# Kernel tuning notes

Measured on AMD Instinct MI355X. Metric: run time of the kernel, lower is better.

The kernel has to match this reference:

```python
import jax, jax.numpy as jnp
import numpy as np


def setup_inputs() -> dict:
    key = jax.random.key(0)
    k1, k2, k3, k4 = jax.random.split(key, 4)
    B, h, w, z, C = 4, 16, 16, 16, 128
    Cq = C // 8
    x = jax.random.normal(k1, (B, h, w, z, C), dtype=jnp.float32)
    # 1x1x1 Conv3D kernels == per-voxel linear projections (he_normal scale)
    Wb = jax.random.normal(k2, (C, Cq), dtype=jnp.float32) * np.sqrt(2.0 / C)
    Wc = jax.random.normal(k3, (C, Cq), dtype=jnp.float32) * np.sqrt(2.0 / C)
    Wd = jax.random.normal(k4, (C, C), dtype=jnp.float32) * np.sqrt(2.0 / C)
    gamma = jnp.zeros((1,), dtype=jnp.float32)
    return {"x": x, "Wb": Wb, "Wc": Wc, "Wd": Wd, "gamma": gamma}


def reference(x, Wb, Wc, Wd, gamma):
    B, h, w, z, C = x.shape
    N = h * w * z
    # 1x1x1 convs = channel projections
    b = jnp.einsum('bhwzc,cf->bhwzf', x, Wb).reshape(B, N, -1)   # [B,N,C/8]
    c = jnp.einsum('bhwzc,cf->bhwzf', x, Wc).reshape(B, N, -1)   # [B,N,C/8]
    d = jnp.einsum('bhwzc,cf->bhwzf', x, Wd).reshape(B, N, C)    # [B,N,C]
    # full NxN attention scores, softmax over last axis (keras softmax default)
    scores = jnp.einsum('bnf,bmf->bnm', b, c)                    # [B,N,N]
    attn = jax.nn.softmax(scores, axis=-1)
    out = jnp.einsum('bnm,bmc->bnc', attn, d).reshape(B, h, w, z, C)
    return gamma * out + x
```

## Files before the change

kernel.cpp:

```cpp
#include <hip/hip_runtime.h>

#define NB     4
#define NN     4096
#define NC     128
#define NCQ    16
#define NROWS  (NB * NN)
#define NSLICE 4
#define NIT    (NN / 64 / NSLICE)

typedef __attribute__((ext_vector_type(8)))  __bf16 bf16x8;
typedef __attribute__((ext_vector_type(4)))  float  f32x4;
typedef __attribute__((ext_vector_type(16))) float  f32x16;

#define MFMA16(a,b,c) __builtin_amdgcn_mfma_f32_16x16x32_bf16((a),(b),(c),0,0,0)
#define MFMA32(a,b,c) __builtin_amdgcn_mfma_f32_32x32x16_bf16((a),(b),(c),0,0,0)
#define LOG2E 1.44269504f
#define SCH_BIAS 16248.66f

__device__ __forceinline__ f32x16 zero16() {
    f32x16 v;
    #pragma unroll
    for (int i = 0; i < 16; ++i) v[i] = 0.f;
    return v;
}


__global__ void wtrans_kernel(const float* __restrict__ Wb,
                              const float* __restrict__ Wc,
                              const float* __restrict__ Wd,
                              __bf16* __restrict__ wtg)
{
    int oc = blockIdx.x;
    int ch = threadIdx.x;
    float v;
    if      (oc < 16) v = Wb[ch * 16  + oc];
    else if (oc < 32) v = Wc[ch * 16  + (oc - 16)];
    else              v = Wd[ch * 128 + (oc - 32)];
    wtg[oc * 128 + ch] = (__bf16)v;
}

__global__ __launch_bounds__(256) void proj_kernel(
    const float* __restrict__ x, const __bf16* __restrict__ wtg,
    __bf16* __restrict__ qswz, __bf16* __restrict__ kswz, __bf16* __restrict__ vswz)
{
    __shared__ __align__(16) __bf16 xsh[32 * 136];
    __shared__ __align__(16) __bf16 wt [160 * 136];
    __shared__ __align__(16) float  osb[4][16 * 17];

    const int  t    = threadIdx.x;
    const int  lane = t & 63, w = t >> 6;
    const int  q16  = lane & 15, quad = lane >> 4;
    const long row0 = (long)blockIdx.x * 32;
    const int  batch = (int)(row0 >> 12);
    const int  nloc  = (int)(row0 & 4095);
    const int  rh   = w & 1;
    const int  og   = (w >> 1) * 5;

    #pragma unroll
    for (int i = 0; i < 4; ++i) {
        int idx = t + 256 * i;
        int r = idx >> 5, c4 = (idx & 31) * 4;
        float4 xv = *(const float4*)&x[(row0 + r) * NC + c4];
        union { __bf16 h[4]; uint2 u; } cv;
        cv.h[0] = (__bf16)xv.x; cv.h[1] = (__bf16)xv.y;
        cv.h[2] = (__bf16)xv.z; cv.h[3] = (__bf16)xv.w;
        *(uint2*)&xsh[r * 136 + c4] = cv.u;
    }
    #pragma unroll
    for (int i = 0; i < 10; ++i) {
        int idx = t + 256 * i;
        int oc = idx >> 4, seg = idx & 15;
        *(uint4*)&wt[oc * 136 + seg * 8] = ((const uint4*)wtg)[idx];
    }
    __syncthreads();

    bf16x8 xf[4];
    #pragma unroll
    for (int kc = 0; kc < 4; ++kc)
        xf[kc] = *(const bf16x8*)&xsh[(rh * 16 + q16) * 136 + kc * 32 + quad * 8];

    float* osw = osb[w];
    #pragma unroll
    for (int oc_t = 0; oc_t < 5; ++oc_t) {
        const int oset = og + oc_t;
        f32x4 acc = {0.f, 0.f, 0.f, 0.f};
        #pragma unroll
        for (int kc = 0; kc < 4; ++kc) {
            bf16x8 wf = *(const bf16x8*)&wt[(oset * 16 + q16) * 136 + kc * 32 + quad * 8];
            acc = MFMA16(wf, xf[kc], acc);
        }
        #pragma unroll
        for (int r = 0; r < 4; ++r)
            osw[(quad * 4 + r) * 17 + q16] = acc[r];

        if (oset >= 2) {
            int ch_l = lane & 15, lh_t = (lane >> 4) & 1, jh = lane >> 5;
            union { __bf16 h[4]; uint2 u; } cv;
            #pragma unroll
            for (int u2 = 0; u2 < 4; ++u2)
                cv.h[u2] = (__bf16)osw[ch_l * 17 + 8 * jh + 4 * lh_t + u2];
            int kb16 = (nloc >> 4) + rh;
            int cg   = (oset - 2) >> 1;
            int l31v = ((oset - 2) & 1) * 16 + ch_l;
            size_t off = ((((size_t)batch * 256 + kb16) * 4 + cg) << 9)
                       + (size_t)(lh_t * 32 + l31v) * 8 + jh * 4;
            *(uint2*)&vswz[off] = cv.u;
        } else if (lane < 32) {
            int xr = lane & 15, lh_t = lane >> 4;
            const float qsc = (oset == 0) ? LOG2E : 1.f;
            union { __bf16 h[8]; uint4 u; } cv;
            #pragma unroll
            for (int j = 0; j < 8; ++j)
                cv.h[j] = (__bf16)(osw[(8 * lh_t + j) * 17 + xr] * qsc);
            size_t off = ((((size_t)batch * 128 + (nloc >> 5)) * 64)
                       + (size_t)(lh_t * 32 + rh * 16 + xr)) * 8;
            __bf16* dst = (oset == 0) ? qswz : kswz;
            *(uint4*)&dst[off] = cv.u;
        }
    }
}

__global__ __launch_bounds__(256, 3) void attn_kernel(
    const __bf16* __restrict__ qswz, const __bf16* __restrict__ kswz,
    const __bf16* __restrict__ vswz, __bf16* __restrict__ Opart,
    float* __restrict__ lws)
{
    const int t    = threadIdx.x;
    const int lane = t & 63, w = t >> 6;
    const int l31 = lane & 31, lh = lane >> 5;
    const int bid   = blockIdx.x;
    const int xcd   = bid & 7;
    const int batch = xcd >> 1;
    const int sp    = xcd & 1;
    const int qb32  = bid >> 3;
    const int h     = w & 1;
    const int slice = sp * 2 + (w >> 1);
    const int ks0   = slice * (64 * NIT);

    const bf16x8 qf = *(const bf16x8*)
        &qswz[(((size_t)batch * 128 + qb32) * 64 + lane) * 8];

    const __bf16* kptr = kswz + ((size_t)batch * 128 + (ks0 >> 5)) * 512 + lane * 8;
    const __bf16* vptr = vswz + ((size_t)batch * 256 + (ks0 >> 4)) * 2048
                       + h * 1024 + lane * 8;

    union { uint32_t u[4]; bf16x8 f; } onesu;
    #pragma unroll
    for (int i = 0; i < 4; ++i) onesu.u[i] = 0x3F803F80u;
    const bf16x8 ones = onesu.f;

    f32x16 O0 = zero16(), O1 = zero16(), Ol = zero16();

    bf16x8 kf0 = *(const bf16x8*)(kptr);
    bf16x8 kf1 = *(const bf16x8*)(kptr + 512);
    bf16x8 va[8], vb[8];
    #pragma unroll
    for (int b = 0; b < 4; ++b) {
        va[2*b]     = *(const bf16x8*)(vptr + (size_t)(b * 4)     * 512);
        va[2*b + 1] = *(const bf16x8*)(vptr + (size_t)(b * 4 + 1) * 512);
    }
    f32x16 S0 = MFMA32(kf0, qf, zero16());
    f32x16 S1 = MFMA32(kf1, qf, zero16());

#define ATTN_BODY(IT, CUR, NXT)                                               \
    {                                                                         \
        const int itn = ((IT) + 1 < NIT) ? (IT) + 1 : (IT);                   \
        kf0 = *(const bf16x8*)(kptr + (size_t)itn * 1024);                    \
        kf1 = *(const bf16x8*)(kptr + (size_t)itn * 1024 + 512);              \
        _Pragma("unroll")                                                     \
        for (int b = 0; b < 4; ++b) {                                         \
            NXT[2*b]     = *(const bf16x8*)(vptr + (size_t)((itn*4+b)*4)*512);\
            NXT[2*b + 1] = *(const bf16x8*)(vptr + (size_t)((itn*4+b)*4+1)*512);\
        }                                                                     \
        union { uint32_t u32[16]; bf16x8 f[4]; } pk;                          \
        _Pragma("unroll")                                                     \
        for (int i = 0; i < 8; ++i) {                                         \
            int e0 = (int)fmaf(S0[2*i],   128.f, SCH_BIAS);                   \
            int e1 = (int)fmaf(S0[2*i+1], 128.f, SCH_BIAS);                   \
            int e2 = (int)fmaf(S1[2*i],   128.f, SCH_BIAS);                   \
            int e3 = (int)fmaf(S1[2*i+1], 128.f, SCH_BIAS);                   \
            pk.u32[i]     = (uint32_t)((e1 << 16) | e0);                      \
            pk.u32[8 + i] = (uint32_t)((e3 << 16) | e2);                      \
        }                                                                     \
        _Pragma("unroll")                                                     \
        for (int b = 0; b < 4; ++b) {                                         \
            O0 = MFMA32(pk.f[b], CUR[2*b],     O0);                           \
            O1 = MFMA32(pk.f[b], CUR[2*b + 1], O1);                           \
            Ol = MFMA32(pk.f[b], ones,         Ol);                           \
        }                                                                     \
        S0 = MFMA32(kf0, qf, zero16());                                       \
        S1 = MFMA32(kf1, qf, zero16());                                       \
    }

    for (int it = 0; it < NIT; it += 2) {
        ATTN_BODY(it,     va, vb);
        ATTN_BODY(it + 1, vb, va);
    }
#undef ATTN_BODY

    const long base = (long)batch * NN;

    if (h == 0 && l31 == 0) {
        #pragma unroll
        for (int r = 0; r < 16; ++r) {
            int q = qb32 * 32 + (r & 3) + 8 * (r >> 2) + 4 * lh;
            lws[(size_t)slice * NROWS + base + q] = Ol[r];
        }
    }

    #pragma unroll
    for (int ct = 0; ct < 2; ++ct) {
        f32x16 Ov = ct ? O1 : O0;
        #pragma unroll
        for (int r = 0; r < 16; ++r) {
            int q = qb32 * 32 + (r & 3) + 8 * (r >> 2) + 4 * lh;
            Opart[((size_t)slice * NROWS + base + q) * NC + 64 * h + 32 * ct + l31]
                = (__bf16)Ov[r];
        }
    }
}

__global__ __launch_bounds__(256) void combine_kernel(
    const __bf16* __restrict__ Op, const float* __restrict__ lws,
    const float* __restrict__ x, const float* __restrict__ gamma,
    float* __restrict__ out)
{
    __shared__ float gl[32];
    const int  t    = threadIdx.x;
    const long row0 = (long)blockIdx.x * 32;
    if (t < 32) {
        float l = 0.f;
        #pragma unroll
        for (int s = 0; s < NSLICE; ++s) l += lws[(size_t)s * NROWS + row0 + t];
        gl[t] = gamma[0] / l;
    }
    __syncthreads();
    const size_t s1 = (size_t)NROWS * NC;
    #pragma unroll
    for (int i = 0; i < 4; ++i) {
        int idx = t + 256 * i;
        int r = idx >> 5, c4 = (idx & 31) * 4;
        size_t g = (size_t)(row0 + r) * NC + c4;
        float a0 = 0.f, a1 = 0.f, a2 = 0.f, a3 = 0.f;
        #pragma unroll
        for (int s = 0; s < NSLICE; ++s) {
            union { __bf16 h[4]; uint2 u; } a;
            a.u = *(const uint2*)&Op[s1 * s + g];
            a0 += (float)a.h[0]; a1 += (float)a.h[1];
            a2 += (float)a.h[2]; a3 += (float)a.h[3];
        }
        float sc = gl[r];
        float4 xv = *(const float4*)&x[g];
        float4 o;
        o.x = a0 * sc + xv.x; o.y = a1 * sc + xv.y;
        o.z = a2 * sc + xv.z; o.w = a3 * sc + xv.w;
        *(float4*)&out[g] = o;
    }
}

extern "C" void kernel_launch(void* const* d_in, const int* in_sizes, int n_in,
                              void* d_out, int out_size, void* d_ws, size_t ws_size,
                              hipStream_t stream) {
    const float* x     = (const float*)d_in[0];
    const float* Wb    = (const float*)d_in[1];
    const float* Wc    = (const float*)d_in[2];
    const float* Wd    = (const float*)d_in[3];
    const float* gamma = (const float*)d_in[4];
    float*       out   = (float*)d_out;

    __bf16* qswz  = (__bf16*)d_ws;
    __bf16* kswz  = qswz + (size_t)NROWS * NCQ;
    __bf16* vswz  = kswz + (size_t)NROWS * NCQ;
    __bf16* wtg   = vswz + (size_t)NB * NC * NN;
    __bf16* Opart = wtg + 160 * 128;
    float*  lws   = (float*)(Opart + (size_t)NSLICE * NROWS * NC);

    wtrans_kernel <<<160, 128, 0, stream>>>(Wb, Wc, Wd, wtg);
    proj_kernel   <<<NROWS / 32, 256, 0, stream>>>(x, wtg, qswz, kswz, vswz);
    attn_kernel   <<<NB * 128 * 2, 256, 0, stream>>>(qswz, kswz, vswz, Opart, lws);
    combine_kernel<<<NROWS / 32, 256, 0, stream>>>(Opart, lws, x, gamma, out);
}
```

Before: 112.8 us.

## Fuse weight transpose into projection and combine into attention via completion counter

Removes the separate weight-transpose kernel: each projection block now reads the fp32 weights directly and transposes and converts them into shared memory. The combine kernel is also removed. Each attention block bumps a per-query-tile atomic counter after writing its partials, and the second block to finish reduces the slices and writes the output. This cuts the launch count from four to two at the cost of redundant weight loads per projection block, strided shared-memory stores, and an atomic plus fences in the attention epilogue.

```diff
diff --git a/kernel.cpp b/kernel.cpp
--- a/kernel.cpp
+++ b/kernel.cpp
@@ -25,23 +25,11 @@
 }
 
 
-__global__ void wtrans_kernel(const float* __restrict__ Wb,
-                              const float* __restrict__ Wc,
-                              const float* __restrict__ Wd,
-                              __bf16* __restrict__ wtg)
-{
-    int oc = blockIdx.x;
-    int ch = threadIdx.x;
-    float v;
-    if      (oc < 16) v = Wb[ch * 16  + oc];
-    else if (oc < 32) v = Wc[ch * 16  + (oc - 16)];
-    else              v = Wd[ch * 128 + (oc - 32)];
-    wtg[oc * 128 + ch] = (__bf16)v;
-}
-
 __global__ __launch_bounds__(256) void proj_kernel(
-    const float* __restrict__ x, const __bf16* __restrict__ wtg,
-    __bf16* __restrict__ qswz, __bf16* __restrict__ kswz, __bf16* __restrict__ vswz)
+    const float* __restrict__ x,  const float* __restrict__ Wb,
+    const float* __restrict__ Wc, const float* __restrict__ Wd,
+    __bf16* __restrict__ qswz, __bf16* __restrict__ kswz,
+    __bf16* __restrict__ vswz, int* __restrict__ cnt)
 {
     __shared__ __align__(16) __bf16 xsh[32 * 136];
     __shared__ __align__(16) __bf16 wt [160 * 136];
@@ -56,6 +44,8 @@
     const int  rh   = w & 1;
     const int  og   = (w >> 1) * 5;
 
+    if (t == 0) cnt[blockIdx.x] = 0;
+
     #pragma unroll
     for (int i = 0; i < 4; ++i) {
         int idx = t + 256 * i;
@@ -67,10 +57,34 @@
         *(uint2*)&xsh[r * 136 + c4] = cv.u;
     }
     #pragma unroll
-    for (int i = 0; i < 10; ++i) {
+    for (int i = 0; i < 2; ++i) {
         int idx = t + 256 * i;
-        int oc = idx >> 4, seg = idx & 15;
-        *(uint4*)&wt[oc * 136 + seg * 8] = ((const uint4*)wtg)[idx];
+        int ch = idx >> 2, o4 = (idx & 3) * 4;
+        float4 v = *(const float4*)&Wb[ch * 16 + o4];
+        wt[(o4 + 0) * 136 + ch] = (__bf16)v.x;
+        wt[(o4 + 1) * 136 + ch] = (__bf16)v.y;
+        wt[(o4 + 2) * 136 + ch] = (__bf16)v.z;
+        wt[(o4 + 3) * 136 + ch] = (__bf16)v.w;
+    }
+    #pragma unroll
+    for (int i = 0; i < 2; ++i) {
+        int idx = t + 256 * i;
+        int ch = idx >> 2, o4 = (idx & 3) * 4;
+        float4 v = *(const float4*)&Wc[ch * 16 + o4];
+        wt[(16 + o4 + 0) * 136 + ch] = (__bf16)v.x;
+        wt[(16 + o4 + 1) * 136 + ch] = (__bf16)v.y;
+        wt[(16 + o4 + 2) * 136 + ch] = (__bf16)v.z;
+        wt[(16 + o4 + 3) * 136 + ch] = (__bf16)v.w;
+    }
+    #pragma unroll
+    for (int i = 0; i < 16; ++i) {
+        int idx = t + 256 * i;
+        int ch = idx >> 5, o4 = (idx & 31) * 4;
+        float4 v = *(const float4*)&Wd[ch * 128 + o4];
+        wt[(32 + o4 + 0) * 136 + ch] = (__bf16)v.x;
+        wt[(32 + o4 + 1) * 136 + ch] = (__bf16)v.y;
+        wt[(32 + o4 + 2) * 136 + ch] = (__bf16)v.z;
+        wt[(32 + o4 + 3) * 136 + ch] = (__bf16)v.w;
     }
     __syncthreads();
 
@@ -123,7 +137,9 @@
 __global__ __launch_bounds__(256, 3) void attn_kernel(
     const __bf16* __restrict__ qswz, const __bf16* __restrict__ kswz,
     const __bf16* __restrict__ vswz, __bf16* __restrict__ Opart,
-    float* __restrict__ lws)
+    float* __restrict__ lws, int* __restrict__ cnt,
+    const float* __restrict__ x, const float* __restrict__ gamma,
+    float* __restrict__ out)
 {
     const int t    = threadIdx.x;
     const int lane = t & 63, w = t >> 6;
@@ -218,43 +234,46 @@
                 = (__bf16)Ov[r];
         }
     }
-}
-
-__global__ __launch_bounds__(256) void combine_kernel(
-    const __bf16* __restrict__ Op, const float* __restrict__ lws,
-    const float* __restrict__ x, const float* __restrict__ gamma,
-    float* __restrict__ out)
-{
+
     __shared__ float gl[32];
-    const int  t    = threadIdx.x;
-    const long row0 = (long)blockIdx.x * 32;
-    if (t < 32) {
-        float l = 0.f;
-        #pragma unroll
-        for (int s = 0; s < NSLICE; ++s) l += lws[(size_t)s * NROWS + row0 + t];
-        gl[t] = gamma[0] / l;
-    }
+    __shared__ int doneSh;
     __syncthreads();
-    const size_t s1 = (size_t)NROWS * NC;
-    #pragma unroll
-    for (int i = 0; i < 4; ++i) {
-        int idx = t + 256 * i;
-        int r = idx >> 5, c4 = (idx & 31) * 4;
-        size_t g = (size_t)(row0 + r) * NC + c4;
-        float a0 = 0.f, a1 = 0.f, a2 = 0.f, a3 = 0.f;
-        #pragma unroll
-        for (int s = 0; s < NSLICE; ++s) {
-            union { __bf16 h[4]; uint2 u; } a;
-            a.u = *(const uint2*)&Op[s1 * s + g];
-            a0 += (float)a.h[0]; a1 += (float)a.h[1];
-            a2 += (float)a.h[2]; a3 += (float)a.h[3];
-        }
-        float sc = gl[r];
-        float4 xv = *(const float4*)&x[g];
-        float4 o;
-        o.x = a0 * sc + xv.x; o.y = a1 * sc + xv.y;
-        o.z = a2 * sc + xv.z; o.w = a3 * sc + xv.w;
-        *(float4*)&out[g] = o;
+    __threadfence();
+    if (t == 0)
+        doneSh = atomicAdd(&cnt[batch * 128 + qb32], 1);
+    __syncthreads();
+    if (doneSh == 1) {
+        __threadfence();
+        const long r0g = base + qb32 * 32;
+        if (t < 32) {
+            float l = 0.f;
+            #pragma unroll
+            for (int s = 0; s < NSLICE; ++s)
+                l += lws[(size_t)s * NROWS + r0g + t];
+            gl[t] = gamma[0] / l;
+        }
+        __syncthreads();
+        const size_t s1 = (size_t)NROWS * NC;
+        #pragma unroll
+        for (int i = 0; i < 4; ++i) {
+            int idx2 = t + 256 * i;
+            int r = idx2 >> 5, c4 = (idx2 & 31) * 4;
+            size_t g = (size_t)(r0g + r) * NC + c4;
+            float a0 = 0.f, a1 = 0.f, a2 = 0.f, a3 = 0.f;
+            #pragma unroll
+            for (int s = 0; s < NSLICE; ++s) {
+                union { __bf16 hh[4]; uint2 u; } a;
+                a.u = *(const uint2*)&Opart[s1 * s + g];
+                a0 += (float)a.hh[0]; a1 += (float)a.hh[1];
+                a2 += (float)a.hh[2]; a3 += (float)a.hh[3];
+            }
+            float sc = gl[r];
+            float4 xv = *(const float4*)&x[g];
+            float4 o;
+            o.x = a0 * sc + xv.x; o.y = a1 * sc + xv.y;
+            o.z = a2 * sc + xv.z; o.w = a3 * sc + xv.w;
+            *(float4*)&out[g] = o;
+        }
     }
 }
 
@@ -271,12 +290,12 @@
     __bf16* qswz  = (__bf16*)d_ws;
     __bf16* kswz  = qswz + (size_t)NROWS * NCQ;
     __bf16* vswz  = kswz + (size_t)NROWS * NCQ;
-    __bf16* wtg   = vswz + (size_t)NB * NC * NN;
-    __bf16* Opart = wtg + 160 * 128;
+    __bf16* Opart = vswz + (size_t)NB * NC * NN;
     float*  lws   = (float*)(Opart + (size_t)NSLICE * NROWS * NC);
-
-    wtrans_kernel <<<160, 128, 0, stream>>>(Wb, Wc, Wd, wtg);
-    proj_kernel   <<<NROWS / 32, 256, 0, stream>>>(x, wtg, qswz, kswz, vswz);
-    attn_kernel   <<<NB * 128 * 2, 256, 0, stream>>>(qswz, kswz, vswz, Opart, lws);
-    combine_kernel<<<NROWS / 32, 256, 0, stream>>>(Opart, lws, x, gamma, out);
+    int*    cnt   = (int*)(lws + (size_t)NSLICE * NROWS);
+
+    proj_kernel<<<NROWS / 32, 256, 0, stream>>>(x, Wb, Wc, Wd,
+                                                qswz, kswz, vswz, cnt);
+    attn_kernel<<<NB * 128 * 2, 256, 0, stream>>>(qswz, kswz, vswz, Opart, lws,
+                                                  cnt, x, gamma, out);
 }
```

New measurement: 319.3 us. +183.1%, slower.
